# Kernel optimization log

Measured on AMD Instinct MI355X. Metric: run time of the kernel, lower is better.

## Reference

```python
import jax, jax.numpy as jnp
import numpy as np

# ---- module hyperparameters (match init_kwargs) ----
SPATIAL = (32, 64)          # token grid, N = 32*64 = 2048
D_MODEL = 1024
N_HEADS = 16
HEAD_DIM = D_MODEL // N_HEADS  # 64
THETA = 10000.0
XPOS_SCALE_BASE = SPATIAL[0] * 2  # 64


def _rope_tables():
    """ND rotary (xpos) tables, lucidrains-style.
    Each spatial axis gets head_dim//ndim rotary channels; frequencies are
    interleave-repeated (r=2) to pair with rotate_half. Returns cos, sin,
    xpos scale, each [N, HEAD_DIM] float32."""
    nd = len(SPATIAL)
    dpa = HEAD_DIM // nd  # dims per axis (32)
    freqs_axes, scale_axes = [], []
    for size in SPATIAL:
        inv_freq = 1.0 / (THETA ** (np.arange(0, dpa, 2, dtype=np.float64) / dpa))
        t = np.arange(size, dtype=np.float64)
        f = np.repeat(t[:, None] * inv_freq[None, :], 2, axis=-1)        # [size, dpa]
        sbase = (np.arange(0, dpa, 2, dtype=np.float64) + 0.4 * dpa) / (1.4 * dpa)
        power = (t - size // 2) / XPOS_SCALE_BASE
        sc = np.repeat(sbase[None, :] ** power[:, None], 2, axis=-1)     # [size, dpa]
        freqs_axes.append(f)
        scale_axes.append(sc)
    # broadcast each axis table over the full grid, concat along channel dim
    def grid_concat(tabs):
        parts = []
        for i, tab in enumerate(tabs):
            shp = [1] * nd + [dpa]
            shp[i] = SPATIAL[i]
            parts.append(np.broadcast_to(tab.reshape(shp), tuple(SPATIAL) + (dpa,)))
        return np.concatenate(parts, axis=-1).reshape(-1, HEAD_DIM)  # [N, HEAD_DIM]
    freqs = grid_concat(freqs_axes)
    xscale = grid_concat(scale_axes)
    return (jnp.asarray(np.cos(freqs), jnp.float32),
            jnp.asarray(np.sin(freqs), jnp.float32),
            jnp.asarray(xscale, jnp.float32))


def _rotate_half(x):
    # pairwise rotation: (x1, x2) -> (-x2, x1), interleaved layout
    x = x.reshape(*x.shape[:-1], -1, 2)
    x1, x2 = x[..., 0], x[..., 1]
    return jnp.stack((-x2, x1), axis=-1).reshape(*x.shape[:-2], -1)


def setup_inputs() -> dict:
    key = jax.random.key(0)
    ks = jax.random.split(key, 3)
    B, N = 2, SPATIAL[0] * SPATIAL[1]
    x = jax.random.normal(ks[0], (B, N, D_MODEL), dtype=jnp.float32)
    w_qkv = jax.random.normal(ks[1], (D_MODEL, 3 * D_MODEL), dtype=jnp.float32) * 0.02
    b_qkv = jnp.zeros((3 * D_MODEL,), jnp.float32)
    w_proj = jax.random.normal(ks[2], (D_MODEL, D_MODEL), dtype=jnp.float32) * 0.02
    b_proj = jnp.zeros((D_MODEL,), jnp.float32)
    return {"x": x, "w_qkv": w_qkv, "b_qkv": b_qkv, "w_proj": w_proj, "b_proj": b_proj}


def reference(x, w_qkv, b_qkv, w_proj, b_proj):
    B, N, C = x.shape
    scale = HEAD_DIM ** -0.5
    qkv = (x @ w_qkv + b_qkv).reshape(B, N, 3, N_HEADS, HEAD_DIM)
    qkv = qkv.transpose(2, 0, 3, 1, 4)  # [3, B, H, N, D]
    q, k, v = qkv[0], qkv[1], qkv[2]
    cos, sin, xs = _rope_tables()       # [N, D], broadcast over B,H
    q = (q * cos + _rotate_half(q) * sin) * xs
    k = (k * cos + _rotate_half(k) * sin) / xs
    attn = jax.nn.softmax(jnp.einsum('bhnd,bhmd->bhnm', q, k) * scale, axis=-1)
    out = jnp.einsum('bhnm,bhmd->bhnd', attn, v)
    out = out.transpose(0, 2, 1, 3).reshape(B, N, C)
    return out @ w_proj + b_proj
```

## Files before the change

### kernel.cpp

```cpp
#include <hip/hip_runtime.h>
#include <math.h>

typedef __attribute__((ext_vector_type(8))) _Float16 f16x8;
typedef __attribute__((ext_vector_type(4))) _Float16 f16x4;
typedef __attribute__((ext_vector_type(4))) float f32x4;

#define MFMAH(a, b, c) __builtin_amdgcn_mfma_f32_16x16x32_f16((a), (b), (c), 0, 0, 0)

#define QSCALE 0.18033688011112042f
#define SOFF 4.328085122666891f


__device__ __forceinline__ void gl_lds16(const _Float16* g, _Float16* l) {
    __builtin_amdgcn_global_load_lds(
        (const __attribute__((address_space(1))) unsigned int*)g,
        (__attribute__((address_space(3))) unsigned int*)l, 16, 0, 0);
}

__global__ void prep_kernel(const float* __restrict__ x, const float* __restrict__ w_qkv,
                            const float* __restrict__ w_proj, _Float16* __restrict__ xb,
                            _Float16* __restrict__ wq, _Float16* __restrict__ wp,
                            float* __restrict__ ct, float* __restrict__ st,
                            float* __restrict__ xt) {
    __shared__ float tile[32][33];
    const int b = blockIdx.x, tid = threadIdx.x;
    if (b < 4096) {
        int i = (b * 256 + tid) * 4;
        float4 v = *(const float4*)&x[i];
        f16x4 h = {(_Float16)v.x, (_Float16)v.y, (_Float16)v.z, (_Float16)v.w};
        *(f16x4*)&xb[i] = h;
    } else if (b < 4096 + 3072 + 1024) {
        int t, C;
        const float* src;
        _Float16* dst;
        if (b < 4096 + 3072) { t = b - 4096; C = 3072; src = w_qkv; dst = wq; }
        else                 { t = b - 4096 - 3072; C = 1024; src = w_proj; dst = wp; }
        const int tr = t & 31, tc = t >> 5;
        const int tx = tid & 31, ty = tid >> 5;
#pragma unroll
        for (int yy = 0; yy < 4; ++yy) {
            int r = ty + yy * 8;
            tile[r][tx] = src[(size_t)(tr * 32 + r) * C + tc * 32 + tx];
        }
        __syncthreads();
#pragma unroll
        for (int yy = 0; yy < 4; ++yy) {
            int r = ty + yy * 8;
            dst[(size_t)(tc * 32 + r) * 1024 + tr * 32 + tx] = (_Float16)tile[tx][r];
        }
    } else {
        int i = (b - 8192) * 256 + tid;
        int n = i >> 6, d = i & 63;
        int gi = n >> 6, gj = n & 63;
        int axis = d >> 5;
        int p = (d & 31) >> 1;
        float t = axis ? (float)gj : (float)gi;
        float half = axis ? 32.0f : 16.0f;
        float inv_freq = powf(10000.0f, -(float)p * (1.0f / 16.0f));
        float fr = t * inv_freq;
        float sbase = (2.0f * p + 12.8f) / 44.8f;
        float xs = powf(sbase, (t - half) * (1.0f / 64.0f));
        ct[i] = cosf(fr);
        st[i] = sinf(fr);
        xt[i] = xs;
    }
}

__global__ __launch_bounds__(256) void gemm_qkv_kernel(
    const _Float16* __restrict__ A_g, const _Float16* __restrict__ B_g,
    const float* __restrict__ bias, const float* __restrict__ ctab,
    const float* __restrict__ stab, const float* __restrict__ xtab,
    _Float16* __restrict__ qb, _Float16* __restrict__ kb, _Float16* __restrict__ vt) {
    __shared__ __align__(16) _Float16 Asm[4096];
    __shared__ __align__(16) _Float16 Bsm[4096];

    const int tid = threadIdx.x;
    const int lane = tid & 63, wave = tid >> 6;
    const int quad = lane >> 4, l16 = lane & 15;
    const int wm = wave >> 1, wn = wave & 1;
    const int m0 = blockIdx.x * 128, n0 = blockIdx.y * 128;

    f32x4 zero = {0.f, 0.f, 0.f, 0.f};
    f32x4 acc[4][4];
#pragma unroll
    for (int i = 0; i < 4; ++i)
#pragma unroll
        for (int j = 0; j < 4; ++j) acc[i][j] = zero;

    const int c1t = tid + 256;
    const int row0 = tid >> 2, s0 = tid & 3;
    const int row1 = c1t >> 2, s1 = c1t & 3;
    const int g0 = s0 ^ ((row0 >> 1) & 3);
    const int g1 = s1 ^ ((row1 >> 1) & 3);
    const _Float16* Ap0 = &A_g[(size_t)(m0 + row0) * 1024 + (g0 << 3)];
    const _Float16* Ap1 = &A_g[(size_t)(m0 + row1) * 1024 + (g1 << 3)];
    const _Float16* Bp0 = &B_g[(size_t)(n0 + row0) * 1024 + (g0 << 3)];
    const _Float16* Bp1 = &B_g[(size_t)(n0 + row1) * 1024 + (g1 << 3)];
    _Float16* La0 = &Asm[tid * 8];
    _Float16* La1 = &Asm[c1t * 8];
    _Float16* Lb0 = &Bsm[tid * 8];
    _Float16* Lb1 = &Bsm[c1t * 8];

    const int sw = (l16 >> 1) & 3;

    for (int k0 = 0; k0 < 1024; k0 += 32) {
        __syncthreads();
        gl_lds16(Ap0 + k0, La0);
        gl_lds16(Ap1 + k0, La1);
        gl_lds16(Bp0 + k0, Lb0);
        gl_lds16(Bp1 + k0, Lb1);
        __syncthreads();

        f16x8 af[4], bf[4];
#pragma unroll
        for (int i = 0; i < 4; ++i) {
            af[i] = *(const f16x8*)&Asm[(wm * 64 + i * 16 + l16) * 32 + ((quad ^ sw) << 3)];
            bf[i] = *(const f16x8*)&Bsm[(wn * 64 + i * 16 + l16) * 32 + ((quad ^ sw) << 3)];
        }
#pragma unroll
        for (int i = 0; i < 4; ++i)
#pragma unroll
            for (int j = 0; j < 4; ++j) acc[i][j] = MFMAH(af[i], bf[j], acc[i][j]);
    }

    float bj[4];
#pragma unroll
    for (int j = 0; j < 4; ++j) bj[j] = bias[n0 + wn * 64 + j * 16 + l16];

    if (n0 < 2048) {
#pragma unroll
        for (int i = 0; i < 4; ++i) {
#pragma unroll
            for (int r = 0; r < 4; ++r) {
                const int row = m0 + wm * 64 + i * 16 + quad * 4 + r;
                const int b = row >> 11, nrow = row & 2047;
#pragma unroll
                for (int j = 0; j < 4; ++j) {
                    const int col = n0 + wn * 64 + j * 16 + l16;
                    float v = acc[i][j][r] + bj[j];
                    float partner = __shfl_xor(v, 1);
                    const int hh = (col >> 6) & 15;
                    const int d = col & 63;
                    const size_t o = ((size_t)(b * 16 + hh) * 2048 + nrow) * 64 + d;
                    float rh = (d & 1) ? partner : -partner;
                    const int ti = nrow * 64 + d;
                    float rv = v * ctab[ti] + rh * stab[ti];
                    float xs = xtab[ti];
                    if (col < 1024)
                        qb[o] = (_Float16)(rv * xs * QSCALE);
                    else
                        kb[o] = (_Float16)(rv / xs);
                }
            }
        }
    } else {
#pragma unroll
        for (int i = 0; i < 4; ++i) {
            const int row = m0 + wm * 64 + i * 16 + quad * 4;
            const int b = row >> 11, nrow = row & 2047;
#pragma unroll
            for (int j = 0; j < 4; ++j) {
                const int col = n0 + wn * 64 + j * 16 + l16;
                const int hh = (col >> 6) & 15;
                const int d = col & 63;
                f16x4 pv4;
#pragma unroll
                for (int r = 0; r < 4; ++r) pv4[r] = (_Float16)(acc[i][j][r] + bj[j]);
                *(f16x4*)&vt[((size_t)(b * 16 + hh) * 64 + d) * 2048 + nrow] = pv4;
            }
        }
    }
}

__global__ __launch_bounds__(256) void gemm_proj_kernel(
    const _Float16* __restrict__ A_g, const _Float16* __restrict__ B_g,
    const float* __restrict__ bias, float* __restrict__ out) {
    __shared__ __align__(16) _Float16 Asm[4096];
    __shared__ __align__(16) _Float16 Bsm[2048];

    const int tid = threadIdx.x;
    const int lane = tid & 63, wave = tid >> 6;
    const int quad = lane >> 4, l16 = lane & 15;
    const int wm = wave >> 1, wn = wave & 1;
    const int m0 = blockIdx.x * 128, n0 = blockIdx.y * 64;

    f32x4 zero = {0.f, 0.f, 0.f, 0.f};
    f32x4 acc[4][2];
#pragma unroll
    for (int i = 0; i < 4; ++i)
#pragma unroll
        for (int j = 0; j < 2; ++j) acc[i][j] = zero;

    const int c1t = tid + 256;
    const int row0 = tid >> 2, s0 = tid & 3;
    const int row1 = c1t >> 2, s1 = c1t & 3;
    const int g0 = s0 ^ ((row0 >> 1) & 3);
    const int g1 = s1 ^ ((row1 >> 1) & 3);
    const _Float16* Ap0 = &A_g[(size_t)(m0 + row0) * 1024 + (g0 << 3)];
    const _Float16* Ap1 = &A_g[(size_t)(m0 + row1) * 1024 + (g1 << 3)];
    const _Float16* Bp0 = &B_g[(size_t)(n0 + row0) * 1024 + (g0 << 3)];
    _Float16* La0 = &Asm[tid * 8];
    _Float16* La1 = &Asm[c1t * 8];
    _Float16* Lb0 = &Bsm[tid * 8];

    const int sw = (l16 >> 1) & 3;

    for (int k0 = 0; k0 < 1024; k0 += 32) {
        __syncthreads();
        gl_lds16(Ap0 + k0, La0);
        gl_lds16(Ap1 + k0, La1);
        gl_lds16(Bp0 + k0, Lb0);
        __syncthreads();

        f16x8 af[4], bf[2];
#pragma unroll
        for (int i = 0; i < 4; ++i)
            af[i] = *(const f16x8*)&Asm[(wm * 64 + i * 16 + l16) * 32 + ((quad ^ sw) << 3)];
#pragma unroll
        for (int j = 0; j < 2; ++j)
            bf[j] = *(const f16x8*)&Bsm[(wn * 32 + j * 16 + l16) * 32 + ((quad ^ sw) << 3)];
#pragma unroll
        for (int i = 0; i < 4; ++i)
#pragma unroll
            for (int j = 0; j < 2; ++j) acc[i][j] = MFMAH(af[i], bf[j], acc[i][j]);
    }

    float bj[2];
#pragma unroll
    for (int j = 0; j < 2; ++j) bj[j] = bias[n0 + wn * 32 + j * 16 + l16];
#pragma unroll
    for (int i = 0; i < 4; ++i)
#pragma unroll
        for (int r = 0; r < 4; ++r) {
            const int row = m0 + wm * 64 + i * 16 + quad * 4 + r;
#pragma unroll
            for (int j = 0; j < 2; ++j) {
                const int col = n0 + wn * 32 + j * 16 + l16;
                out[(size_t)row * 1024 + col] = acc[i][j][r] + bj[j];
            }
        }
}

#define KLD 72
#define PLD 72

__global__ __launch_bounds__(256) void attn_kernel(
    const _Float16* __restrict__ qb, const _Float16* __restrict__ kb,
    const _Float16* __restrict__ vt, _Float16* __restrict__ ao) {
    __shared__ __align__(16) _Float16 Ksm0[64 * KLD], Ksm1[64 * KLD];
    __shared__ __align__(16) _Float16 Vsm0[64 * KLD], Vsm1[64 * KLD];
    __shared__ __align__(16) _Float16 Psm[4 * 32 * PLD];

    const int tid = threadIdx.x;
    const int lane = tid & 63, wave = tid >> 6;
    const int quad = lane >> 4, l16 = lane & 15;
    const int bh = blockIdx.x & 31, qt = blockIdx.x >> 5;
    const size_t base = (size_t)bh * 2048 * 64;
    const int qrow0 = qt * 128 + wave * 32;

    f16x8 qf[2][2];
#pragma unroll
    for (int rg = 0; rg < 2; ++rg) {
        qf[rg][0] = *(const f16x8*)&qb[base + (size_t)(qrow0 + rg * 16 + l16) * 64 + quad * 8];
        qf[rg][1] = *(const f16x8*)&qb[base + (size_t)(qrow0 + rg * 16 + l16) * 64 + 32 + quad * 8];
    }

    f32x4 moff = {-SOFF, -SOFF, -SOFF, -SOFF};
    f32x4 zero = {0.f, 0.f, 0.f, 0.f};
    f32x4 o[2][4];
    float lsum[2] = {0.f, 0.f};
#pragma unroll
    for (int rg = 0; rg < 2; ++rg)
#pragma unroll
        for (int dc = 0; dc < 4; ++dc) o[rg][dc] = zero;

    const int kr0 = tid >> 3, ko0 = (tid & 7) << 3;
    const int kr1 = kr0 + 32;
    f16x8 pk0, pk1, pv0, pv1;
    auto gload = [&](int kt) {
        pk0 = *(const f16x8*)&kb[base + (size_t)(kt + kr0) * 64 + ko0];
        pk1 = *(const f16x8*)&kb[base + (size_t)(kt + kr1) * 64 + ko0];
        pv0 = *(const f16x8*)&vt[((size_t)bh * 64 + kr0) * 2048 + kt + ko0];
        pv1 = *(const f16x8*)&vt[((size_t)bh * 64 + kr1) * 2048 + kt + ko0];
    };
    auto stage = [&](_Float16* Ks, _Float16* Vs) {
        *(f16x8*)&Ks[kr0 * KLD + ko0] = pk0;
        *(f16x8*)&Ks[kr1 * KLD + ko0] = pk1;
        *(f16x8*)&Vs[kr0 * KLD + ko0] = pv0;
        *(f16x8*)&Vs[kr1 * KLD + ko0] = pv1;
    };

    _Float16* Pw = &Psm[wave * 32 * PLD];

    auto compute = [&](const _Float16* Ks, const _Float16* Vs) {
        f32x4 s[2][4];
#pragma unroll
        for (int kg = 0; kg < 4; ++kg) {
            f16x8 kf0 = *(const f16x8*)&Ks[(kg * 16 + l16) * KLD + quad * 8];
            f16x8 kf1 = *(const f16x8*)&Ks[(kg * 16 + l16) * KLD + 32 + quad * 8];
            s[0][kg] = MFMAH(kf0, qf[0][0], moff);
            s[0][kg] = MFMAH(kf1, qf[0][1], s[0][kg]);
            s[1][kg] = MFMAH(kf0, qf[1][0], moff);
            s[1][kg] = MFMAH(kf1, qf[1][1], s[1][kg]);
        }
#pragma unroll
        for (int rg = 0; rg < 2; ++rg)
#pragma unroll
            for (int kg = 0; kg < 4; ++kg) {
                float p0 = __builtin_amdgcn_exp2f(s[rg][kg][0]);
                float p1 = __builtin_amdgcn_exp2f(s[rg][kg][1]);
                float p2 = __builtin_amdgcn_exp2f(s[rg][kg][2]);
                float p3 = __builtin_amdgcn_exp2f(s[rg][kg][3]);
                lsum[rg] += (p0 + p1) + (p2 + p3);
                f16x4 ph = {(_Float16)p0, (_Float16)p1, (_Float16)p2, (_Float16)p3};
                *(f16x4*)&Pw[(rg * 16 + l16) * PLD + kg * 16 + quad * 4] = ph;
            }
        f16x8 pf[2][2];
#pragma unroll
        for (int rg = 0; rg < 2; ++rg) {
            pf[rg][0] = *(const f16x8*)&Pw[(rg * 16 + l16) * PLD + quad * 8];
            pf[rg][1] = *(const f16x8*)&Pw[(rg * 16 + l16) * PLD + 32 + quad * 8];
        }
#pragma unroll
        for (int dc = 0; dc < 4; ++dc) {
            f16x8 vf0 = *(const f16x8*)&Vs[(dc * 16 + l16) * KLD + quad * 8];
            f16x8 vf1 = *(const f16x8*)&Vs[(dc * 16 + l16) * KLD + 32 + quad * 8];
#pragma unroll
            for (int rg = 0; rg < 2; ++rg) {
                o[rg][dc] = MFMAH(pf[rg][0], vf0, o[rg][dc]);
                o[rg][dc] = MFMAH(pf[rg][1], vf1, o[rg][dc]);
            }
        }
    };

    gload(0);
    stage(Ksm0, Vsm0);
    gload(64);
    __syncthreads();

    for (int it = 0; it < 32; it += 2) {
        stage(Ksm1, Vsm1);
        if (it + 2 < 32) gload((it + 2) * 64);
        compute(Ksm0, Vsm0);
        __syncthreads();
        if (it + 2 < 32) stage(Ksm0, Vsm0);
        if (it + 3 < 32) gload((it + 3) * 64);
        compute(Ksm1, Vsm1);
        __syncthreads();
    }

    float linv[2][4];
#pragma unroll
    for (int rg = 0; rg < 2; ++rg) {
        float v = lsum[rg];
        v += __shfl_xor(v, 16);
        v += __shfl_xor(v, 32);
        v = 1.0f / v;
#pragma unroll
        for (int r = 0; r < 4; ++r) linv[rg][r] = __shfl(v, quad * 4 + r);
    }

    const int b = bh >> 4, hh = bh & 15;
#pragma unroll
    for (int rg = 0; rg < 2; ++rg)
#pragma unroll
        for (int dc = 0; dc < 4; ++dc)
#pragma unroll
            for (int r = 0; r < 4; ++r) {
                float v = o[rg][dc][r] * linv[rg][r];
                const int qrow = qrow0 + rg * 16 + quad * 4 + r;
                const size_t oi = ((size_t)(b * 2048 + qrow)) * 1024 + hh * 64 + dc * 16 + l16;
                ao[oi] = (_Float16)v;
            }
}

extern "C" void kernel_launch(void* const* d_in, const int* in_sizes, int n_in,
                              void* d_out, int out_size, void* d_ws, size_t ws_size,
                              hipStream_t stream) {
    const float* x = (const float*)d_in[0];
    const float* w_qkv = (const float*)d_in[1];
    const float* b_qkv = (const float*)d_in[2];
    const float* w_proj = (const float*)d_in[3];
    const float* b_proj = (const float*)d_in[4];
    float* out = (float*)d_out;

    char* ws = (char*)d_ws;
    size_t off = 0;
    auto take = [&](size_t bytes) { char* p = ws + off; off += bytes; return p; };
    _Float16* xbuf   = (_Float16*)take(8388608);
    _Float16* wqkvT  = (_Float16*)take(6291456);
    _Float16* wprojT = (_Float16*)take(2097152);
    _Float16* qbuf   = (_Float16*)take(8388608);
    _Float16* kbuf   = (_Float16*)take(8388608);
    _Float16* vtbuf  = (_Float16*)take(8388608);
    float* ctab      = (float*)take(524288);
    float* stab      = (float*)take(524288);
    float* xtab      = (float*)take(524288);
    _Float16* ao = xbuf;

    prep_kernel<<<8704, 256, 0, stream>>>(x, w_qkv, w_proj, xbuf, wqkvT, wprojT,
                                          ctab, stab, xtab);
    gemm_qkv_kernel<<<dim3(32, 24), 256, 0, stream>>>(xbuf, wqkvT, b_qkv,
                                                      ctab, stab, xtab, qbuf, kbuf, vtbuf);
    attn_kernel<<<512, 256, 0, stream>>>(qbuf, kbuf, vtbuf, ao);
    gemm_proj_kernel<<<dim3(32, 16), 256, 0, stream>>>(ao, wprojT, b_proj, out);
}
```

Before: 193.9 us.

## Load K/V MFMA fragments directly from global into registers, drop LDS staging

The attention kernel no longer stages K and V tiles through double-buffered shared memory with block-wide barriers. Each wave now loads its K and V MFMA operand fragments straight from global memory into registers, prefetching the next tile during the current tile's softmax. This removes the LDS writes and reads and the __syncthreads calls. In exchange, each of the four waves fetches the same K/V data separately, which quadruples global/L2 traffic and raises register pressure.

```diff
diff --git a/kernel.cpp b/kernel.cpp
--- a/kernel.cpp
+++ b/kernel.cpp
@@ -241,14 +241,11 @@
         }
 }
 
-#define KLD 72
 #define PLD 72
 
 __global__ __launch_bounds__(256) void attn_kernel(
     const _Float16* __restrict__ qb, const _Float16* __restrict__ kb,
     const _Float16* __restrict__ vt, _Float16* __restrict__ ao) {
-    __shared__ __align__(16) _Float16 Ksm0[64 * KLD], Ksm1[64 * KLD];
-    __shared__ __align__(16) _Float16 Vsm0[64 * KLD], Vsm1[64 * KLD];
     __shared__ __align__(16) _Float16 Psm[4 * 32 * PLD];
 
     const int tid = threadIdx.x;
@@ -274,34 +271,41 @@
 #pragma unroll
         for (int dc = 0; dc < 4; ++dc) o[rg][dc] = zero;
 
-    const int kr0 = tid >> 3, ko0 = (tid & 7) << 3;
-    const int kr1 = kr0 + 32;
-    f16x8 pk0, pk1, pv0, pv1;
-    auto gload = [&](int kt) {
-        pk0 = *(const f16x8*)&kb[base + (size_t)(kt + kr0) * 64 + ko0];
-        pk1 = *(const f16x8*)&kb[base + (size_t)(kt + kr1) * 64 + ko0];
-        pv0 = *(const f16x8*)&vt[((size_t)bh * 64 + kr0) * 2048 + kt + ko0];
-        pv1 = *(const f16x8*)&vt[((size_t)bh * 64 + kr1) * 2048 + kt + ko0];
+    const _Float16* Kp = &kb[base + (size_t)l16 * 64 + quad * 8];
+    const _Float16* Vp = &vt[((size_t)bh * 64 + l16) * 2048 + quad * 8];
+
+    f16x8 kf[4][2], vfA[4][2], vfB[4][2];
+    auto loadK = [&](int kt) {
+#pragma unroll
+        for (int kg = 0; kg < 4; ++kg) {
+            const _Float16* p = Kp + (size_t)(kt + kg * 16) * 64;
+            kf[kg][0] = *(const f16x8*)p;
+            kf[kg][1] = *(const f16x8*)(p + 32);
+        }
     };
-    auto stage = [&](_Float16* Ks, _Float16* Vs) {
-        *(f16x8*)&Ks[kr0 * KLD + ko0] = pk0;
-        *(f16x8*)&Ks[kr1 * KLD + ko0] = pk1;
-        *(f16x8*)&Vs[kr0 * KLD + ko0] = pv0;
-        *(f16x8*)&Vs[kr1 * KLD + ko0] = pv1;
+    auto loadV = [&](f16x8 (&vf)[4][2], int kt) {
+#pragma unroll
+        for (int dc = 0; dc < 4; ++dc) {
+            const _Float16* p = Vp + (size_t)(dc * 16) * 2048 + kt;
+            vf[dc][0] = *(const f16x8*)p;
+            vf[dc][1] = *(const f16x8*)(p + 32);
+        }
     };
 
     _Float16* Pw = &Psm[wave * 32 * PLD];
 
-    auto compute = [&](const _Float16* Ks, const _Float16* Vs) {
+    auto tile = [&](f16x8 (&vf)[4][2], f16x8 (&vfn)[4][2], int t) {
         f32x4 s[2][4];
 #pragma unroll
         for (int kg = 0; kg < 4; ++kg) {
-            f16x8 kf0 = *(const f16x8*)&Ks[(kg * 16 + l16) * KLD + quad * 8];
-            f16x8 kf1 = *(const f16x8*)&Ks[(kg * 16 + l16) * KLD + 32 + quad * 8];
-            s[0][kg] = MFMAH(kf0, qf[0][0], moff);
-            s[0][kg] = MFMAH(kf1, qf[0][1], s[0][kg]);
-            s[1][kg] = MFMAH(kf0, qf[1][0], moff);
-            s[1][kg] = MFMAH(kf1, qf[1][1], s[1][kg]);
+            s[0][kg] = MFMAH(kf[kg][0], qf[0][0], moff);
+            s[0][kg] = MFMAH(kf[kg][1], qf[0][1], s[0][kg]);
+            s[1][kg] = MFMAH(kf[kg][0], qf[1][0], moff);
+            s[1][kg] = MFMAH(kf[kg][1], qf[1][1], s[1][kg]);
+        }
+        if (t + 1 < 32) {
+            loadK((t + 1) * 64);
+            loadV(vfn, (t + 1) * 64);
         }
 #pragma unroll
         for (int rg = 0; rg < 2; ++rg)
@@ -322,31 +326,19 @@
             pf[rg][1] = *(const f16x8*)&Pw[(rg * 16 + l16) * PLD + 32 + quad * 8];
         }
 #pragma unroll
-        for (int dc = 0; dc < 4; ++dc) {
-            f16x8 vf0 = *(const f16x8*)&Vs[(dc * 16 + l16) * KLD + quad * 8];
-            f16x8 vf1 = *(const f16x8*)&Vs[(dc * 16 + l16) * KLD + 32 + quad * 8];
+        for (int dc = 0; dc < 4; ++dc)
 #pragma unroll
             for (int rg = 0; rg < 2; ++rg) {
-                o[rg][dc] = MFMAH(pf[rg][0], vf0, o[rg][dc]);
-                o[rg][dc] = MFMAH(pf[rg][1], vf1, o[rg][dc]);
-            }
-        }
+                o[rg][dc] = MFMAH(pf[rg][0], vf[dc][0], o[rg][dc]);
+                o[rg][dc] = MFMAH(pf[rg][1], vf[dc][1], o[rg][dc]);
+            }
     };
 
-    gload(0);
-    stage(Ksm0, Vsm0);
-    gload(64);
-    __syncthreads();
-
-    for (int it = 0; it < 32; it += 2) {
-        stage(Ksm1, Vsm1);
-        if (it + 2 < 32) gload((it + 2) * 64);
-        compute(Ksm0, Vsm0);
-        __syncthreads();
-        if (it + 2 < 32) stage(Ksm0, Vsm0);
-        if (it + 3 < 32) gload((it + 3) * 64);
-        compute(Ksm1, Vsm1);
-        __syncthreads();
+    loadK(0);
+    loadV(vfA, 0);
+    for (int t = 0; t < 32; t += 2) {
+        tile(vfA, vfB, t);
+        tile(vfB, vfA, t + 1);
     }
 
     float linv[2][4];
```

Measured after the change: 263.2 us. 35.7% more time.

## Switch attention to 32x32x16 MFMA and pass P via lane shuffles instead of LDS

Applied to the files above, without the earlier changes.

Rewrites the attention inner loop to use 32x32x16 f16 MFMA tiles, computing S^T so each lane holds a column of probabilities. The probabilities are converted to f16 and exchanged between lane halves with cross-lane shuffles to form the PV operand directly, removing the per-wave P scratch buffer in LDS and its store/load round trip. This halves the MFMA instruction count and removes LDS traffic, at the cost of more shuffle and select instructions and larger accumulator register usage.

```diff
diff --git a/kernel.cpp b/kernel.cpp
--- a/kernel.cpp
+++ b/kernel.cpp
@@ -4,8 +4,10 @@
 typedef __attribute__((ext_vector_type(8))) _Float16 f16x8;
 typedef __attribute__((ext_vector_type(4))) _Float16 f16x4;
 typedef __attribute__((ext_vector_type(4))) float f32x4;
+typedef __attribute__((ext_vector_type(16))) float f32x16;
 
 #define MFMAH(a, b, c) __builtin_amdgcn_mfma_f32_16x16x32_f16((a), (b), (c), 0, 0, 0)
+#define MFMA32(a, b, c) __builtin_amdgcn_mfma_f32_32x32x16_f16((a), (b), (c), 0, 0, 0)
 
 #define QSCALE 0.18033688011112042f
 #define SOFF 4.328085122666891f
@@ -15,6 +17,13 @@
     __builtin_amdgcn_global_load_lds(
         (const __attribute__((address_space(1))) unsigned int*)g,
         (__attribute__((address_space(3))) unsigned int*)l, 16, 0, 0);
+}
+
+__device__ __forceinline__ unsigned pkh(float a, float b) {
+    union { _Float16 h[2]; unsigned u; } x;
+    x.h[0] = (_Float16)a;
+    x.h[1] = (_Float16)b;
+    return x.u;
 }
 
 __global__ void prep_kernel(const float* __restrict__ x, const float* __restrict__ w_qkv,
@@ -242,37 +251,30 @@
 }
 
 #define KLD 72
-#define PLD 72
 
 __global__ __launch_bounds__(256) void attn_kernel(
     const _Float16* __restrict__ qb, const _Float16* __restrict__ kb,
     const _Float16* __restrict__ vt, _Float16* __restrict__ ao) {
     __shared__ __align__(16) _Float16 Ksm0[64 * KLD], Ksm1[64 * KLD];
     __shared__ __align__(16) _Float16 Vsm0[64 * KLD], Vsm1[64 * KLD];
-    __shared__ __align__(16) _Float16 Psm[4 * 32 * PLD];
 
     const int tid = threadIdx.x;
     const int lane = tid & 63, wave = tid >> 6;
-    const int quad = lane >> 4, l16 = lane & 15;
+    const int l32 = lane & 31, hi = lane >> 5, hi8 = hi << 3;
     const int bh = blockIdx.x & 31, qt = blockIdx.x >> 5;
     const size_t base = (size_t)bh * 2048 * 64;
     const int qrow0 = qt * 128 + wave * 32;
 
-    f16x8 qf[2][2];
-#pragma unroll
-    for (int rg = 0; rg < 2; ++rg) {
-        qf[rg][0] = *(const f16x8*)&qb[base + (size_t)(qrow0 + rg * 16 + l16) * 64 + quad * 8];
-        qf[rg][1] = *(const f16x8*)&qb[base + (size_t)(qrow0 + rg * 16 + l16) * 64 + 32 + quad * 8];
-    }
-
-    f32x4 moff = {-SOFF, -SOFF, -SOFF, -SOFF};
-    f32x4 zero = {0.f, 0.f, 0.f, 0.f};
-    f32x4 o[2][4];
-    float lsum[2] = {0.f, 0.f};
-#pragma unroll
-    for (int rg = 0; rg < 2; ++rg)
-#pragma unroll
-        for (int dc = 0; dc < 4; ++dc) o[rg][dc] = zero;
+    f16x8 qf[4];
+#pragma unroll
+    for (int dc = 0; dc < 4; ++dc)
+        qf[dc] = *(const f16x8*)&qb[base + (size_t)(qrow0 + l32) * 64 + dc * 16 + hi8];
+
+    f32x16 moff16, zero16;
+#pragma unroll
+    for (int e = 0; e < 16; ++e) { moff16[e] = -SOFF; zero16[e] = 0.f; }
+    f32x16 o0 = zero16, o1 = zero16;
+    float lsum = 0.f;
 
     const int kr0 = tid >> 3, ko0 = (tid & 7) << 3;
     const int kr1 = kr0 + 32;
@@ -290,46 +292,47 @@
         *(f16x8*)&Vs[kr1 * KLD + ko0] = pv1;
     };
 
-    _Float16* Pw = &Psm[wave * 32 * PLD];
-
     auto compute = [&](const _Float16* Ks, const _Float16* Vs) {
-        f32x4 s[2][4];
-#pragma unroll
-        for (int kg = 0; kg < 4; ++kg) {
-            f16x8 kf0 = *(const f16x8*)&Ks[(kg * 16 + l16) * KLD + quad * 8];
-            f16x8 kf1 = *(const f16x8*)&Ks[(kg * 16 + l16) * KLD + 32 + quad * 8];
-            s[0][kg] = MFMAH(kf0, qf[0][0], moff);
-            s[0][kg] = MFMAH(kf1, qf[0][1], s[0][kg]);
-            s[1][kg] = MFMAH(kf0, qf[1][0], moff);
-            s[1][kg] = MFMAH(kf1, qf[1][1], s[1][kg]);
-        }
-#pragma unroll
-        for (int rg = 0; rg < 2; ++rg)
-#pragma unroll
-            for (int kg = 0; kg < 4; ++kg) {
-                float p0 = __builtin_amdgcn_exp2f(s[rg][kg][0]);
-                float p1 = __builtin_amdgcn_exp2f(s[rg][kg][1]);
-                float p2 = __builtin_amdgcn_exp2f(s[rg][kg][2]);
-                float p3 = __builtin_amdgcn_exp2f(s[rg][kg][3]);
-                lsum[rg] += (p0 + p1) + (p2 + p3);
-                f16x4 ph = {(_Float16)p0, (_Float16)p1, (_Float16)p2, (_Float16)p3};
-                *(f16x4*)&Pw[(rg * 16 + l16) * PLD + kg * 16 + quad * 4] = ph;
-            }
-        f16x8 pf[2][2];
-#pragma unroll
-        for (int rg = 0; rg < 2; ++rg) {
-            pf[rg][0] = *(const f16x8*)&Pw[(rg * 16 + l16) * PLD + quad * 8];
-            pf[rg][1] = *(const f16x8*)&Pw[(rg * 16 + l16) * PLD + 32 + quad * 8];
-        }
+        f32x16 s0 = moff16, s1 = moff16;
 #pragma unroll
         for (int dc = 0; dc < 4; ++dc) {
-            f16x8 vf0 = *(const f16x8*)&Vs[(dc * 16 + l16) * KLD + quad * 8];
-            f16x8 vf1 = *(const f16x8*)&Vs[(dc * 16 + l16) * KLD + 32 + quad * 8];
-#pragma unroll
-            for (int rg = 0; rg < 2; ++rg) {
-                o[rg][dc] = MFMAH(pf[rg][0], vf0, o[rg][dc]);
-                o[rg][dc] = MFMAH(pf[rg][1], vf1, o[rg][dc]);
-            }
+            f16x8 kf0 = *(const f16x8*)&Ks[l32 * KLD + dc * 16 + hi8];
+            f16x8 kf1 = *(const f16x8*)&Ks[(32 + l32) * KLD + dc * 16 + hi8];
+            s0 = MFMA32(kf0, qf[dc], s0);
+            s1 = MFMA32(kf1, qf[dc], s1);
+        }
+        float p0[16], p1[16];
+#pragma unroll
+        for (int e = 0; e < 16; ++e) {
+            p0[e] = __builtin_amdgcn_exp2f(s0[e]);
+            lsum += p0[e];
+        }
+#pragma unroll
+        for (int e = 0; e < 16; ++e) {
+            p1[e] = __builtin_amdgcn_exp2f(s1[e]);
+            lsum += p1[e];
+        }
+#pragma unroll
+        for (int c = 0; c < 4; ++c) {
+            const float* ps = (c < 2) ? p0 : p1;
+            const int bo = (c & 1) * 8;
+            unsigned lo0 = pkh(ps[bo + 0], ps[bo + 1]);
+            unsigned lo1 = pkh(ps[bo + 2], ps[bo + 3]);
+            unsigned hi0 = pkh(ps[bo + 4], ps[bo + 5]);
+            unsigned hi1 = pkh(ps[bo + 6], ps[bo + 7]);
+            unsigned send0 = hi ? lo0 : hi0;
+            unsigned send1 = hi ? lo1 : hi1;
+            unsigned r0 = (unsigned)__shfl_xor((int)send0, 32);
+            unsigned r1 = (unsigned)__shfl_xor((int)send1, 32);
+            union { unsigned w[4]; f16x8 v; } pf;
+            pf.w[0] = hi ? r0 : lo0;
+            pf.w[1] = hi ? r1 : lo1;
+            pf.w[2] = hi ? hi0 : r0;
+            pf.w[3] = hi ? hi1 : r1;
+            f16x8 vf0 = *(const f16x8*)&Vs[l32 * KLD + c * 16 + hi8];
+            f16x8 vf1 = *(const f16x8*)&Vs[(32 + l32) * KLD + c * 16 + hi8];
+            o0 = MFMA32(pf.v, vf0, o0);
+            o1 = MFMA32(pf.v, vf1, o1);
         }
     };
 
@@ -349,29 +352,21 @@
         __syncthreads();
     }
 
-    float linv[2][4];
-#pragma unroll
-    for (int rg = 0; rg < 2; ++rg) {
-        float v = lsum[rg];
-        v += __shfl_xor(v, 16);
-        v += __shfl_xor(v, 32);
-        v = 1.0f / v;
-#pragma unroll
-        for (int r = 0; r < 4; ++r) linv[rg][r] = __shfl(v, quad * 4 + r);
-    }
+    float vsum = lsum + __shfl_xor(lsum, 32);
+    float vinv = 1.0f / vsum;
+    float linv[16];
+#pragma unroll
+    for (int r = 0; r < 16; ++r)
+        linv[r] = __shfl(vinv, (r & 3) + 8 * (r >> 2) + 4 * hi);
 
     const int b = bh >> 4, hh = bh & 15;
 #pragma unroll
-    for (int rg = 0; rg < 2; ++rg)
-#pragma unroll
-        for (int dc = 0; dc < 4; ++dc)
-#pragma unroll
-            for (int r = 0; r < 4; ++r) {
-                float v = o[rg][dc][r] * linv[rg][r];
-                const int qrow = qrow0 + rg * 16 + quad * 4 + r;
-                const size_t oi = ((size_t)(b * 2048 + qrow)) * 1024 + hh * 64 + dc * 16 + l16;
-                ao[oi] = (_Float16)v;
-            }
+    for (int r = 0; r < 16; ++r) {
+        const int qrow = qrow0 + (r & 3) + 8 * (r >> 2) + 4 * hi;
+        const size_t oi = ((size_t)(b * 2048 + qrow)) * 1024 + hh * 64 + l32;
+        ao[oi] = (_Float16)(o0[r] * linv[r]);
+        ao[oi + 32] = (_Float16)(o1[r] * linv[r]);
+    }
 }
 
 extern "C" void kernel_launch(void* const* d_in, const int* in_sizes, int n_in,
```

After: 198.2 us. 2.2% more time.
